# Kernel optimization log

Measured on AMD Instinct MI355X. Metric: run time of the kernel, lower is better.

## Reference

```python
import math
import jax, jax.numpy as jnp
import numpy as np

B, T, E, H = 2, 2048, 1024, 16
HS = E // H  # head size = 64
NEG = jnp.float32(-1e10)


def setup_inputs() -> dict:
    key = jax.random.key(0)
    ks = jax.random.split(key, 7)
    return {
        "query": jax.random.normal(ks[0], (B, T, E), jnp.float32),
        "key": jax.random.normal(ks[1], (B, T, E), jnp.float32),
        "value": jax.random.normal(ks[2], (B, T, E), jnp.float32),
        "Wq": jax.random.normal(ks[3], (E, E), jnp.float32) * 0.02,
        "Wk": jax.random.normal(ks[4], (E, E), jnp.float32) * 0.02,
        "Wv": jax.random.normal(ks[5], (E, E), jnp.float32) * 0.02,
        "Wp": jax.random.normal(ks[6], (E, E), jnp.float32) * 0.02,
    }


def reference(query, key, value, Wq, Wk, Wv, Wp):
    # QKV projections (no bias), split into heads: [B, H, T, HS]
    q = (query @ Wq).reshape(B, T, H, HS).transpose(0, 2, 1, 3)
    k = (key @ Wk).reshape(B, T, H, HS).transpose(0, 2, 1, 3)
    v = (value @ Wv).reshape(B, T, H, HS).transpose(0, 2, 1, 3)
    # scaled dot-product scores [B, H, T, T]
    att = jnp.einsum("bhqd,bhkd->bhqk", q, k) / math.sqrt(HS)
    # additive causal mask (tril allowed)
    causal = jnp.tril(jnp.ones((T, T), dtype=att.dtype))
    att = att + jnp.where(causal == 0, NEG, jnp.float32(0.0))[None, None]
    att = jax.nn.softmax(att, axis=-1)
    # dropout rate 0 / deterministic -> identity
    y = jnp.einsum("bhqk,bhkd->bhqd", att, v)
    y = y.transpose(0, 2, 1, 3).reshape(B, T, E)
    y = y @ Wp
    return y
```

## Files before the change

### kernel.cpp

```cpp
#include <hip/hip_runtime.h>

#define TB 2
#define TT 2048
#define TE 1024
#define TH 16
#define THS 64
#define TM (TB * TT)

typedef __attribute__((ext_vector_type(8))) short short8;
typedef __attribute__((ext_vector_type(4))) float f32x4;

__device__ __forceinline__ f32x4 mfma16(short8 a, short8 b, f32x4 c) {
    return __builtin_amdgcn_mfma_f32_16x16x32_bf16(a, b, c, 0, 0, 0);
}

__device__ __forceinline__ void gload_lds16(const void* g, void* l) {
    __builtin_amdgcn_global_load_lds(
        (const __attribute__((address_space(1))) void*)g,
        (__attribute__((address_space(3))) void*)l, 16, 0, 0);
}

__device__ __forceinline__ unsigned short f2bf(float f) {
    unsigned int u = __float_as_uint(f);
    u += 0x7fff + ((u >> 16) & 1);
    return (unsigned short)(u >> 16);
}

__global__ __launch_bounds__(256) void cast3_f32_bf16(
    const float* __restrict__ a, const float* __restrict__ b,
    const float* __restrict__ c, unsigned short* __restrict__ oa,
    unsigned short* __restrict__ ob, unsigned short* __restrict__ oc, int n4) {
    const float* src = (blockIdx.y == 0) ? a : (blockIdx.y == 1) ? b : c;
    unsigned short* dst = (blockIdx.y == 0) ? oa : (blockIdx.y == 1) ? ob : oc;
    int i = blockIdx.x * 256 + threadIdx.x;
    if (i < n4) {
        float4 v = ((const float4*)src)[i];
        ushort4 o;
        o.x = f2bf(v.x); o.y = f2bf(v.y); o.z = f2bf(v.z); o.w = f2bf(v.w);
        ((ushort4*)dst)[i] = o;
    }
}

__global__ __launch_bounds__(256) void transpose_cast_w4(
    const float* __restrict__ W0, const float* __restrict__ W1,
    const float* __restrict__ W2, const float* __restrict__ W3,
    unsigned short* __restrict__ T0, unsigned short* __restrict__ T1,
    unsigned short* __restrict__ T2, unsigned short* __restrict__ T3) {
    __shared__ float Ts[32][33];
    const int z = blockIdx.z;
    const float* W = (z == 0) ? W0 : (z == 1) ? W1 : (z == 2) ? W2 : W3;
    unsigned short* Wt = (z == 0) ? T0 : (z == 1) ? T1 : (z == 2) ? T2 : T3;
    const int r0 = blockIdx.y * 32, c0 = blockIdx.x * 32;
    const int t = threadIdx.x;
    const int r = t >> 3, c = (t & 7) * 4;
    float4 v = *(const float4*)&W[(size_t)(r0 + r) * TE + c0 + c];
    Ts[r][c] = v.x; Ts[r][c + 1] = v.y; Ts[r][c + 2] = v.z; Ts[r][c + 3] = v.w;
    __syncthreads();
    ushort4 o;
    o.x = f2bf(Ts[c + 0][r]); o.y = f2bf(Ts[c + 1][r]);
    o.z = f2bf(Ts[c + 2][r]); o.w = f2bf(Ts[c + 3][r]);
    *(ushort4*)&Wt[(size_t)(c0 + r) * TE + r0 + c] = o;
}

__global__ __launch_bounds__(256, 4) void gemm_qkv(
    const unsigned short* __restrict__ qc, const unsigned short* __restrict__ kc,
    const unsigned short* __restrict__ vc, const unsigned short* __restrict__ Wqt,
    const unsigned short* __restrict__ Wkt, const unsigned short* __restrict__ Wvt,
    unsigned short* __restrict__ Qb, unsigned short* __restrict__ Kb,
    unsigned short* __restrict__ Vt) {
    __shared__ unsigned short As[2][64 * 32];
    __shared__ unsigned short Bs[2][128 * 32];

    const int z = blockIdx.z;
    const unsigned short* A  = (z == 0) ? qc : (z == 1) ? kc : vc;
    const unsigned short* Bt = (z == 0) ? Wqt : (z == 1) ? Wkt : Wvt;

    const int tid = threadIdx.x;
    const int w = tid >> 6, lane = tid & 63;
    const int quad = lane >> 4, l16 = lane & 15;
    const int bm = blockIdx.x * 64, bn = blockIdx.y * 128;
    const int wm = (w >> 1) * 32, wn = (w & 1) * 64;

    f32x4 acc[2][4];
    const f32x4 fz = {0.f, 0.f, 0.f, 0.f};
    #pragma unroll
    for (int i = 0; i < 2; ++i)
        #pragma unroll
        for (int j = 0; j < 4; ++j) acc[i][j] = fz;

    const int srow = lane >> 2;
    const int scol = (((lane & 3) ^ ((srow >> 1) & 3))) * 8;
    const int rchunk = (quad ^ ((l16 >> 1) & 3)) * 8;

    auto stage = [&](int k0, int buf) {
        #pragma unroll
        for (int i = 0; i < 3; ++i) {
            const int ch = w * 3 + i;
            if (ch < 4)
                gload_lds16(A + (size_t)(bm + ch * 16 + srow) * TE + k0 + scol,
                            &As[buf][ch * 512 + lane * 8]);
            else
                gload_lds16(Bt + (size_t)(bn + (ch - 4) * 16 + srow) * TE + k0 + scol,
                            &Bs[buf][(ch - 4) * 512 + lane * 8]);
        }
    };

    stage(0, 0);
    int cur = 0;
    for (int k0 = 0; k0 < TE; k0 += 32) {
        __syncthreads();
        if (k0 + 32 < TE) stage(k0 + 32, cur ^ 1);

        short8 af[2], bf[4];
        #pragma unroll
        for (int i = 0; i < 2; ++i)
            af[i] = *(const short8*)&As[cur][(wm + i * 16 + l16) * 32 + rchunk];
        #pragma unroll
        for (int j = 0; j < 4; ++j)
            bf[j] = *(const short8*)&Bs[cur][(wn + j * 16 + l16) * 32 + rchunk];
        #pragma unroll
        for (int i = 0; i < 2; ++i)
            #pragma unroll
            for (int j = 0; j < 4; ++j)
                acc[i][j] = mfma16(af[i], bf[j], acc[i][j]);
        cur ^= 1;
    }

    if (z < 2) {
        unsigned short* Cb = (z == 0) ? Qb : Kb;
        #pragma unroll
        for (int i = 0; i < 2; ++i)
            #pragma unroll
            for (int j = 0; j < 4; ++j) {
                const int m0 = bm + wm + i * 16 + quad * 4;
                const int n = bn + wn + j * 16 + l16;
                #pragma unroll
                for (int r = 0; r < 4; ++r)
                    Cb[(size_t)(m0 + r) * TE + n] = f2bf(acc[i][j][r]);
            }
    } else {
        #pragma unroll
        for (int i = 0; i < 2; ++i)
            #pragma unroll
            for (int j = 0; j < 4; ++j) {
                const int m0 = bm + wm + i * 16 + quad * 4;
                const int n = bn + wn + j * 16 + l16;
                ushort4 o;
                o.x = f2bf(acc[i][j][0]); o.y = f2bf(acc[i][j][1]);
                o.z = f2bf(acc[i][j][2]); o.w = f2bf(acc[i][j][3]);
                size_t idx = ((size_t)((m0 >> 11) * TH + (n >> 6)) * THS + (n & 63)) * TT + (m0 & (TT - 1));
                *(ushort4*)&Vt[idx] = o;
            }
    }
}

__global__ __launch_bounds__(256, 4) void gemm_out(
    const unsigned short* __restrict__ A, const unsigned short* __restrict__ Bt,
    float* __restrict__ C) {
    __shared__ unsigned short As[2][64 * 32];
    __shared__ unsigned short Bs[2][64 * 32];

    const int tid = threadIdx.x;
    const int w = tid >> 6, lane = tid & 63;
    const int quad = lane >> 4, l16 = lane & 15;
    const int bm = blockIdx.x * 64, bn = blockIdx.y * 64;
    const int wm = (w >> 1) * 32, wn = (w & 1) * 32;

    f32x4 acc[2][2];
    const f32x4 fz = {0.f, 0.f, 0.f, 0.f};
    #pragma unroll
    for (int i = 0; i < 2; ++i)
        #pragma unroll
        for (int j = 0; j < 2; ++j) acc[i][j] = fz;

    const int srow = lane >> 2;
    const int scol = (((lane & 3) ^ ((srow >> 1) & 3))) * 8;
    const int rchunk = (quad ^ ((l16 >> 1) & 3)) * 8;

    auto stage = [&](int k0, int buf) {
        #pragma unroll
        for (int i = 0; i < 2; ++i) {
            const int ch = w * 2 + i;
            if (ch < 4)
                gload_lds16(A + (size_t)(bm + ch * 16 + srow) * TE + k0 + scol,
                            &As[buf][ch * 512 + lane * 8]);
            else
                gload_lds16(Bt + (size_t)(bn + (ch - 4) * 16 + srow) * TE + k0 + scol,
                            &Bs[buf][(ch - 4) * 512 + lane * 8]);
        }
    };

    stage(0, 0);
    int cur = 0;
    for (int k0 = 0; k0 < TE; k0 += 32) {
        __syncthreads();
        if (k0 + 32 < TE) stage(k0 + 32, cur ^ 1);

        short8 af[2], bf[2];
        #pragma unroll
        for (int i = 0; i < 2; ++i)
            af[i] = *(const short8*)&As[cur][(wm + i * 16 + l16) * 32 + rchunk];
        #pragma unroll
        for (int j = 0; j < 2; ++j)
            bf[j] = *(const short8*)&Bs[cur][(wn + j * 16 + l16) * 32 + rchunk];
        #pragma unroll
        for (int i = 0; i < 2; ++i)
            #pragma unroll
            for (int j = 0; j < 2; ++j)
                acc[i][j] = mfma16(af[i], bf[j], acc[i][j]);
        cur ^= 1;
    }

    #pragma unroll
    for (int i = 0; i < 2; ++i)
        #pragma unroll
        for (int j = 0; j < 2; ++j) {
            const int m0 = bm + wm + i * 16 + quad * 4;
            const int n = bn + wn + j * 16 + l16;
            #pragma unroll
            for (int r = 0; r < 4; ++r)
                C[(size_t)(m0 + r) * TE + n] = acc[i][j][r];
        }
}

__global__ __launch_bounds__(256, 4) void attn_mfma(
    const unsigned short* __restrict__ Q, const unsigned short* __restrict__ K,
    const unsigned short* __restrict__ Vt, unsigned short* __restrict__ O) {
    __shared__ unsigned short Ks[2][2 * 64 * 32];
    __shared__ unsigned short Vs[2][2 * 64 * 32];

    const int tid = threadIdx.x;
    const int w = tid >> 6, lane = tid & 63;
    const int quad = lane >> 4, l16 = lane & 15;
    const int p = blockIdx.x;
    const int bh = blockIdx.y;
    const int b = bh >> 4, h = bh & 15;
    const int itA = (TT / 64) - 1 - p;
    const int itB = p;

    const unsigned short* Kg = K + (size_t)b * TT * TE + h * THS;
    const unsigned short* Vg = Vt + (size_t)bh * THS * TT;

    const size_t qrowA = (size_t)(b * TT + itA * 64 + w * 16 + l16) * TE + h * THS;
    const size_t qrowB = (size_t)(b * TT + itB * 64 + w * 16 + l16) * TE + h * THS;
    const short8 aqA0 = *(const short8*)&Q[qrowA + quad * 8];
    const short8 aqA1 = *(const short8*)&Q[qrowA + 32 + quad * 8];
    const short8 aqB0 = *(const short8*)&Q[qrowB + quad * 8];
    const short8 aqB1 = *(const short8*)&Q[qrowB + 32 + quad * 8];

    const f32x4 fz = {0.f, 0.f, 0.f, 0.f};
    const int srow = lane >> 2;
    const int scol = (((lane & 3) ^ ((srow >> 1) & 3))) * 8;
    const int rchunk = (quad ^ ((l16 >> 1) & 3)) * 8;

    auto stageKV = [&](int jt, int buf) {
        const int k0 = jt * 64;
        if (w < 2) {
            #pragma unroll
            for (int j = 0; j < 4; ++j) {
                const int ee = w * 4 + j;
                const int kk = ee >> 2, r16 = (ee & 3) * 16;
                gload_lds16(Kg + (size_t)(k0 + r16 + srow) * TE + kk * 32 + scol,
                            &Ks[buf][ee * 512 + lane * 8]);
            }
        } else {
            #pragma unroll
            for (int j = 0; j < 4; ++j) {
                const int ee = (w - 2) * 4 + j;
                const int kk = ee >> 2, r16 = (ee & 3) * 16;
                gload_lds16(Vg + (size_t)(r16 + srow) * TT + k0 + kk * 32 + scol,
                            &Vs[buf][ee * 512 + lane * 8]);
            }
        }
    };

    int cur = 0;
    const float SC = 0.18033688011112042f;
    const int src0 = ((quad & 1) << 5) + l16;
    const bool hi = quad >= 2;

    auto segment = [&](int it, short8 aq0, short8 aq1, bool prefetch_next_seg) {
        f32x4 acc_o[4];
        #pragma unroll
        for (int ni = 0; ni < 4; ++ni) acc_o[ni] = fz;
        float lacc = 0.f;
        const int q0 = it * 64;
        const int qg = q0 + w * 16 + l16;

        for (int jt = 0; jt <= it; ++jt) {
            __syncthreads();
            if (jt < it) stageKV(jt + 1, cur ^ 1);
            else if (prefetch_next_seg) stageKV(0, cur ^ 1);

            f32x4 s[4];
            #pragma unroll
            for (int ni = 0; ni < 4; ++ni) {
                short8 kf0 = *(const short8*)&Ks[cur][(ni * 16 + l16) * 32 + rchunk];
                short8 kf1 = *(const short8*)&Ks[cur][2048 + (ni * 16 + l16) * 32 + rchunk];
                s[ni] = mfma16(kf0, aq0, fz);
                s[ni] = mfma16(kf1, aq1, s[ni]);
            }

            const int k0 = jt * 64;
            float pv[4][4];
            if (jt == it) {
                #pragma unroll
                for (int ni = 0; ni < 4; ++ni) {
                    const int kpb = k0 + ni * 16 + quad * 4;
                    #pragma unroll
                    for (int r = 0; r < 4; ++r) {
                        float sv = (kpb + r > qg) ? -1e30f : s[ni][r] * SC;
                        pv[ni][r] = __builtin_amdgcn_exp2f(sv);
                        lacc += pv[ni][r];
                    }
                }
            } else {
                #pragma unroll
                for (int ni = 0; ni < 4; ++ni)
                    #pragma unroll
                    for (int r = 0; r < 4; ++r) {
                        pv[ni][r] = __builtin_amdgcn_exp2f(s[ni][r] * SC);
                        lacc += pv[ni][r];
                    }
            }

            unsigned int pd0[4], pd1[4];
            #pragma unroll
            for (int t = 0; t < 4; ++t) {
                pd0[t] = (unsigned)f2bf(pv[t][0]) | ((unsigned)f2bf(pv[t][1]) << 16);
                pd1[t] = (unsigned)f2bf(pv[t][2]) | ((unsigned)f2bf(pv[t][3]) << 16);
            }

            short8 pf[2];
            #pragma unroll
            for (int c = 0; c < 2; ++c) {
                const int tl = 2 * c, th = 2 * c + 1;
                unsigned d0l = __shfl(pd0[tl], src0),      d0h = __shfl(pd0[th], src0);
                unsigned d1l = __shfl(pd1[tl], src0),      d1h = __shfl(pd1[th], src0);
                unsigned d2l = __shfl(pd0[tl], src0 + 16), d2h = __shfl(pd0[th], src0 + 16);
                unsigned d3l = __shfl(pd1[tl], src0 + 16), d3h = __shfl(pd1[th], src0 + 16);
                union { unsigned u[4]; short8 s8; } pk;
                pk.u[0] = hi ? d0h : d0l;
                pk.u[1] = hi ? d1h : d1l;
                pk.u[2] = hi ? d2h : d2l;
                pk.u[3] = hi ? d3h : d3l;
                pf[c] = pk.s8;
            }

            #pragma unroll
            for (int ni = 0; ni < 4; ++ni) {
                short8 v0 = *(const short8*)&Vs[cur][(ni * 16 + l16) * 32 + rchunk];
                short8 v1 = *(const short8*)&Vs[cur][2048 + (ni * 16 + l16) * 32 + rchunk];
                acc_o[ni] = mfma16(pf[0], v0, acc_o[ni]);
                acc_o[ni] = mfma16(pf[1], v1, acc_o[ni]);
            }
            cur ^= 1;
        }

        lacc += __shfl_xor(lacc, 16);
        lacc += __shfl_xor(lacc, 32);
        float linv[4];
        #pragma unroll
        for (int r = 0; r < 4; ++r)
            linv[r] = 1.0f / __shfl(lacc, quad * 4 + r);

        unsigned short* Og = O + (size_t)(b * TT + q0 + w * 16 + quad * 4) * TE + h * THS;
        #pragma unroll
        for (int r = 0; r < 4; ++r)
            #pragma unroll
            for (int ni = 0; ni < 4; ++ni)
                Og[(size_t)r * TE + ni * 16 + l16] = f2bf(acc_o[ni][r] * linv[r]);
    };

    stageKV(0, 0);
    segment(itA, aqA0, aqA1, true);
    segment(itB, aqB0, aqB1, false);
}

extern "C" void kernel_launch(void* const* d_in, const int* in_sizes, int n_in,
                              void* d_out, int out_size, void* d_ws, size_t ws_size,
                              hipStream_t stream) {
    const float* q  = (const float*)d_in[0];
    const float* k  = (const float*)d_in[1];
    const float* v  = (const float*)d_in[2];
    const float* Wq = (const float*)d_in[3];
    const float* Wk = (const float*)d_in[4];
    const float* Wv = (const float*)d_in[5];
    const float* Wp = (const float*)d_in[6];
    float* out = (float*)d_out;

    const size_t se = (size_t)TM * TE;
    unsigned short* qc  = (unsigned short*)d_ws;
    unsigned short* kc  = qc + se;
    unsigned short* vc  = kc + se;
    unsigned short* Qb  = vc + se;
    unsigned short* Kb  = Qb + se;
    unsigned short* Vt  = Kb + se;
    unsigned short* Ob  = Vt + se;
    unsigned short* Wqt = Ob + se;
    unsigned short* Wkt = Wqt + (size_t)TE * TE;
    unsigned short* Wvt = Wkt + (size_t)TE * TE;
    unsigned short* Wpt = Wvt + (size_t)TE * TE;

    const int n4 = (int)(se / 4);
    cast3_f32_bf16<<<dim3(n4 / 256, 3), 256, 0, stream>>>(q, k, v, qc, kc, vc, n4);
    transpose_cast_w4<<<dim3(TE / 32, TE / 32, 4), 256, 0, stream>>>(
        Wq, Wk, Wv, Wp, Wqt, Wkt, Wvt, Wpt);

    gemm_qkv<<<dim3(TM / 64, TE / 128, 3), 256, 0, stream>>>(
        qc, kc, vc, Wqt, Wkt, Wvt, Qb, Kb, Vt);

    attn_mfma<<<dim3(TT / 64 / 2, TB * TH), 256, 0, stream>>>(Qb, Kb, Vt, Ob);

    gemm_out<<<dim3(TM / 64, TE / 64), 256, 0, stream>>>(Ob, Wpt, out);
}
```

Measured before the change: 220.6 us.

## Split attention KV range across two wave groups per block and merge in LDS

The attention kernel now runs 512 threads per block. Two groups of four waves each process half of the key/value tiles for the same query tiles, and their partial outputs and row sums are merged through LDS at the end. This shortens the serial KV loop per wave, which should lower latency on the long causal rows. The block index is also remapped so that consecutive blocks cover different heads. The cost is double LDS use, an extra merge and synchronization step, and some wasted masked tiles when a tile count is odd.

```diff
diff --git a/kernel.cpp b/kernel.cpp
--- a/kernel.cpp
+++ b/kernel.cpp
@@ -223,17 +223,22 @@
         }
 }
 
-__global__ __launch_bounds__(256, 4) void attn_mfma(
+__global__ __launch_bounds__(512, 4) void attn_mfma(
     const unsigned short* __restrict__ Q, const unsigned short* __restrict__ K,
     const unsigned short* __restrict__ Vt, unsigned short* __restrict__ O) {
-    __shared__ unsigned short Ks[2][2 * 64 * 32];
-    __shared__ unsigned short Vs[2][2 * 64 * 32];
+    __shared__ unsigned short S[2][16384];
+    __shared__ float L0[64];
 
     const int tid = threadIdx.x;
-    const int w = tid >> 6, lane = tid & 63;
+    const int lane = tid & 63;
+    const int wv = tid >> 6;
+    const int wk = wv >> 2;
+    const int wl = wv & 3;
     const int quad = lane >> 4, l16 = lane & 15;
-    const int p = blockIdx.x;
-    const int bh = blockIdx.y;
+
+    const int lin = blockIdx.x;
+    const int bh = (lin & 7) * 4 + ((lin >> 3) & 3);
+    const int p = lin >> 5;
     const int b = bh >> 4, h = bh & 15;
     const int itA = (TT / 64) - 1 - p;
     const int itB = p;
@@ -241,35 +246,38 @@
     const unsigned short* Kg = K + (size_t)b * TT * TE + h * THS;
     const unsigned short* Vg = Vt + (size_t)bh * THS * TT;
 
-    const size_t qrowA = (size_t)(b * TT + itA * 64 + w * 16 + l16) * TE + h * THS;
-    const size_t qrowB = (size_t)(b * TT + itB * 64 + w * 16 + l16) * TE + h * THS;
-    const short8 aqA0 = *(const short8*)&Q[qrowA + quad * 8];
-    const short8 aqA1 = *(const short8*)&Q[qrowA + 32 + quad * 8];
-    const short8 aqB0 = *(const short8*)&Q[qrowB + quad * 8];
-    const short8 aqB1 = *(const short8*)&Q[qrowB + 32 + quad * 8];
+    const size_t qrA = (size_t)(b * TT + itA * 64 + wl * 16 + l16) * TE + h * THS;
+    const size_t qrB = (size_t)(b * TT + itB * 64 + wl * 16 + l16) * TE + h * THS;
+    const short8 aqA0 = *(const short8*)&Q[qrA + quad * 8];
+    const short8 aqA1 = *(const short8*)&Q[qrA + 32 + quad * 8];
+    const short8 aqB0 = *(const short8*)&Q[qrB + quad * 8];
+    const short8 aqB1 = *(const short8*)&Q[qrB + 32 + quad * 8];
 
     const f32x4 fz = {0.f, 0.f, 0.f, 0.f};
     const int srow = lane >> 2;
     const int scol = (((lane & 3) ^ ((srow >> 1) & 3))) * 8;
     const int rchunk = (quad ^ ((l16 >> 1) & 3)) * 8;
 
-    auto stageKV = [&](int jt, int buf) {
-        const int k0 = jt * 64;
-        if (w < 2) {
+    unsigned short* Sw = S[wk];
+    float* Sf = (float*)S;
+
+    auto stageKV = [&](int jt, int it, int buf) {
+        const int k0 = (jt > it ? it : jt) * 64;
+        if (wl < 2) {
             #pragma unroll
             for (int j = 0; j < 4; ++j) {
-                const int ee = w * 4 + j;
+                const int ee = wl * 4 + j;
                 const int kk = ee >> 2, r16 = (ee & 3) * 16;
                 gload_lds16(Kg + (size_t)(k0 + r16 + srow) * TE + kk * 32 + scol,
-                            &Ks[buf][ee * 512 + lane * 8]);
+                            &Sw[buf * 4096 + ee * 512 + lane * 8]);
             }
         } else {
             #pragma unroll
             for (int j = 0; j < 4; ++j) {
-                const int ee = (w - 2) * 4 + j;
+                const int ee = (wl - 2) * 4 + j;
                 const int kk = ee >> 2, r16 = (ee & 3) * 16;
                 gload_lds16(Vg + (size_t)(r16 + srow) * TT + k0 + kk * 32 + scol,
-                            &Vs[buf][ee * 512 + lane * 8]);
+                            &Sw[8192 + buf * 4096 + ee * 512 + lane * 8]);
             }
         }
     };
@@ -279,49 +287,43 @@
     const int src0 = ((quad & 1) << 5) + l16;
     const bool hi = quad >= 2;
 
-    auto segment = [&](int it, short8 aq0, short8 aq1, bool prefetch_next_seg) {
+    auto segment = [&](int it, short8 aq0, short8 aq1, int nextit ) {
+        const int h0 = (it + 2) >> 1;
+        const int base = wk ? h0 : 0;
         f32x4 acc_o[4];
         #pragma unroll
         for (int ni = 0; ni < 4; ++ni) acc_o[ni] = fz;
         float lacc = 0.f;
         const int q0 = it * 64;
-        const int qg = q0 + w * 16 + l16;
-
-        for (int jt = 0; jt <= it; ++jt) {
+        const int qg = q0 + wl * 16 + l16;
+
+        for (int i = 0; i < h0; ++i) {
+            const int jt = base + i;
             __syncthreads();
-            if (jt < it) stageKV(jt + 1, cur ^ 1);
-            else if (prefetch_next_seg) stageKV(0, cur ^ 1);
+            if (i + 1 < h0) stageKV(base + i + 1, it, cur ^ 1);
+            else if (nextit >= 0) stageKV(wk ? ((nextit + 2) >> 1) : 0, nextit, cur ^ 1);
 
             f32x4 s[4];
             #pragma unroll
             for (int ni = 0; ni < 4; ++ni) {
-                short8 kf0 = *(const short8*)&Ks[cur][(ni * 16 + l16) * 32 + rchunk];
-                short8 kf1 = *(const short8*)&Ks[cur][2048 + (ni * 16 + l16) * 32 + rchunk];
+                short8 kf0 = *(const short8*)&Sw[cur * 4096 + (ni * 16 + l16) * 32 + rchunk];
+                short8 kf1 = *(const short8*)&Sw[cur * 4096 + 2048 + (ni * 16 + l16) * 32 + rchunk];
                 s[ni] = mfma16(kf0, aq0, fz);
                 s[ni] = mfma16(kf1, aq1, s[ni]);
             }
 
             const int k0 = jt * 64;
+            const int lim = (jt < it) ? 0x7fffffff : ((jt == it) ? qg : -0x7fffffff);
             float pv[4][4];
-            if (jt == it) {
+            #pragma unroll
+            for (int ni = 0; ni < 4; ++ni) {
+                const int kpb = k0 + ni * 16 + quad * 4;
                 #pragma unroll
-                for (int ni = 0; ni < 4; ++ni) {
-                    const int kpb = k0 + ni * 16 + quad * 4;
-                    #pragma unroll
-                    for (int r = 0; r < 4; ++r) {
-                        float sv = (kpb + r > qg) ? -1e30f : s[ni][r] * SC;
-                        pv[ni][r] = __builtin_amdgcn_exp2f(sv);
-                        lacc += pv[ni][r];
-                    }
+                for (int r = 0; r < 4; ++r) {
+                    float sv = (kpb + r > lim) ? -1e30f : s[ni][r] * SC;
+                    pv[ni][r] = __builtin_amdgcn_exp2f(sv);
+                    lacc += pv[ni][r];
                 }
-            } else {
-                #pragma unroll
-                for (int ni = 0; ni < 4; ++ni)
-                    #pragma unroll
-                    for (int r = 0; r < 4; ++r) {
-                        pv[ni][r] = __builtin_amdgcn_exp2f(s[ni][r] * SC);
-                        lacc += pv[ni][r];
-                    }
             }
 
             unsigned int pd0[4], pd1[4];
@@ -349,8 +351,8 @@
 
             #pragma unroll
             for (int ni = 0; ni < 4; ++ni) {
-                short8 v0 = *(const short8*)&Vs[cur][(ni * 16 + l16) * 32 + rchunk];
-                short8 v1 = *(const short8*)&Vs[cur][2048 + (ni * 16 + l16) * 32 + rchunk];
+                short8 v0 = *(const short8*)&Sw[8192 + cur * 4096 + (ni * 16 + l16) * 32 + rchunk];
+                short8 v1 = *(const short8*)&Sw[8192 + cur * 4096 + 2048 + (ni * 16 + l16) * 32 + rchunk];
                 acc_o[ni] = mfma16(pf[0], v0, acc_o[ni]);
                 acc_o[ni] = mfma16(pf[1], v1, acc_o[ni]);
             }
@@ -359,22 +361,43 @@
 
         lacc += __shfl_xor(lacc, 16);
         lacc += __shfl_xor(lacc, 32);
-        float linv[4];
-        #pragma unroll
-        for (int r = 0; r < 4; ++r)
-            linv[r] = 1.0f / __shfl(lacc, quad * 4 + r);
-
-        unsigned short* Og = O + (size_t)(b * TT + q0 + w * 16 + quad * 4) * TE + h * THS;
-        #pragma unroll
-        for (int r = 0; r < 4; ++r)
+
+        __syncthreads();
+        const int fb = cur ^ 1;
+        if (wk == 0) {
             #pragma unroll
             for (int ni = 0; ni < 4; ++ni)
-                Og[(size_t)r * TE + ni * 16 + l16] = f2bf(acc_o[ni][r] * linv[r]);
+                #pragma unroll
+                for (int r = 0; r < 4; ++r) {
+                    const int row = wl * 16 + quad * 4 + r;
+                    const int idx = row * 64 + ni * 16 + l16;
+                    Sf[(idx >> 11) * 8192 + fb * 2048 + (idx & 2047)] = acc_o[ni][r];
+                }
+            if (quad == 0) L0[wl * 16 + l16] = lacc;
+        }
+        __syncthreads();
+        if (wk == 1) {
+            const float lf = lacc + L0[wl * 16 + l16];
+            float linv[4];
+            #pragma unroll
+            for (int r = 0; r < 4; ++r)
+                linv[r] = 1.0f / __shfl(lf, quad * 4 + r);
+            unsigned short* Og = O + (size_t)(b * TT + q0 + wl * 16 + quad * 4) * TE + h * THS;
+            #pragma unroll
+            for (int r = 0; r < 4; ++r)
+                #pragma unroll
+                for (int ni = 0; ni < 4; ++ni) {
+                    const int row = wl * 16 + quad * 4 + r;
+                    const int idx = row * 64 + ni * 16 + l16;
+                    const float o = acc_o[ni][r] + Sf[(idx >> 11) * 8192 + fb * 2048 + (idx & 2047)];
+                    Og[(size_t)r * TE + ni * 16 + l16] = f2bf(o * linv[r]);
+                }
+        }
     };
 
-    stageKV(0, 0);
-    segment(itA, aqA0, aqA1, true);
-    segment(itB, aqB0, aqB1, false);
+    stageKV(wk ? ((itA + 2) >> 1) : 0, itA, 0);
+    segment(itA, aqA0, aqA1, itB);
+    segment(itB, aqB0, aqB1, -1);
 }
 
 extern "C" void kernel_launch(void* const* d_in, const int* in_sizes, int n_in,
@@ -410,7 +433,7 @@
     gemm_qkv<<<dim3(TM / 64, TE / 128, 3), 256, 0, stream>>>(
         qc, kc, vc, Wqt, Wkt, Wvt, Qb, Kb, Vt);
 
-    attn_mfma<<<dim3(TT / 64 / 2, TB * TH), 256, 0, stream>>>(Qb, Kb, Vt, Ob);
+    attn_mfma<<<512, 512, 0, stream>>>(Qb, Kb, Vt, Ob);
 
     gemm_out<<<dim3(TM / 64, TE / 64), 256, 0, stream>>>(Ob, Wpt, out);
 }
```

After: 219.6 us. No clear change (-0.5%).
